# Kernel tuning notes

Hardware: AMD Instinct MI355X
Metric: run time of the kernel (lower is better)

## Reference

```python
import jax, jax.numpy as jnp
import numpy as np

NODE_DIM = 512
HIDDEN = 4096
N_NODES = 4096  # must equal HIDDEN for pool Linear to typecheck (as in source)
N_EDGES = 131072


def setup_inputs() -> dict:
    key = jax.random.key(0)
    ks = jax.random.split(key, 12)
    s1 = 0.02
    x = jax.random.normal(ks[0], (N_NODES, NODE_DIM), dtype=jnp.float32)
    edge_index = jax.random.randint(ks[1], (2, N_EDGES), 0, N_NODES, dtype=jnp.int64)
    # encoder: Linear(node_dim, hidden) -> ReLU -> Linear(hidden, hidden)
    W1 = jax.random.normal(ks[2], (NODE_DIM, HIDDEN), dtype=jnp.float32) * s1
    b1 = jnp.zeros((HIDDEN,), dtype=jnp.float32)
    W2 = jax.random.normal(ks[3], (HIDDEN, HIDDEN), dtype=jnp.float32) * s1
    b2 = jnp.zeros((HIDDEN,), dtype=jnp.float32)
    # pool: Linear(hidden, hidden) -> ReLU -> Linear(hidden, 1)
    W3 = jax.random.normal(ks[4], (HIDDEN, HIDDEN), dtype=jnp.float32) * s1
    b3 = jnp.zeros((HIDDEN,), dtype=jnp.float32)
    W4 = jax.random.normal(ks[5], (HIDDEN, 1), dtype=jnp.float32) * s1
    b4 = jnp.zeros((1,), dtype=jnp.float32)
    return {"x": x, "edge_index": edge_index, "W1": W1, "b1": b1,
            "W2": W2, "b2": b2, "W3": W3, "b3": b3, "W4": W4, "b4": b4}


def reference(x, edge_index, W1, b1, W2, b2, W3, b3, W4, b4):
    # encoder MLP: [N, node_dim] -> [N, hidden]
    h = jax.nn.relu(x @ W1 + b1) @ W2 + b2
    # kernel_vector = (h @ h.T).sum(1) == h @ h.sum(0)  (avoids O(N^2) Gram)
    s = h.sum(axis=0)                 # [hidden]
    kernel_vector = h @ s             # [N]
    kv = kernel_vector[None, :]       # [1, N] with N == hidden
    pooled = jax.nn.relu(kv @ W3 + b3) @ W4 + b4   # [1, 1]
    return pooled
```

## Files before the change

kernel.cpp:

```cpp
#include <hip/hip_runtime.h>

#define NODES 4096
#define NDIM  512
#define HID   4096

typedef __attribute__((ext_vector_type(8))) short bf16x8;
typedef __attribute__((ext_vector_type(4))) float f32x4;

__device__ __forceinline__ float b2f(short v) {
  union { unsigned int u; float f; } c;
  c.u = ((unsigned int)(unsigned short)v) << 16;
  return c.f;
}
__device__ __forceinline__ short f2b(float f) {
  union { float f; unsigned int u; } c; c.f = f;
  unsigned int r = c.u + 0x7fffu + ((c.u >> 16) & 1u);
  return (short)(r >> 16);
}

__global__ __launch_bounds__(256) void k_prep(const float* __restrict__ x,
                                              const float* __restrict__ W1,
                                              const float* __restrict__ b2,
                                              const float* __restrict__ b3,
                                              short* __restrict__ xb,
                                              short* __restrict__ w1t,
                                              float* __restrict__ aacc,
                                              float* __restrict__ svec,
                                              float* __restrict__ uacc) {
  __shared__ float tile[32][33];
  int b = blockIdx.x;
  if (b < 2048) {
    int i = (b * 256 + threadIdx.x) * 4;
    float4 v = *(const float4*)(x + i);
    short4 o;
    o.x = f2b(v.x); o.y = f2b(v.y); o.z = f2b(v.z); o.w = f2b(v.w);
    *(short4*)(xb + i) = o;
  } else if (b < 4096) {
    int t = b - 2048;
    int n0 = (t & 127) * 32;
    int k0 = (t >> 7) * 32;
    int tx = threadIdx.x & 31, ty = threadIdx.x >> 5;
    #pragma unroll
    for (int j = 0; j < 4; ++j) {
      int kk = ty + j * 8;
      tile[kk][tx] = W1[(size_t)(k0 + kk) * HID + n0 + tx];
    }
    __syncthreads();
    #pragma unroll
    for (int j = 0; j < 4; ++j) {
      int nn = ty + j * 8;
      w1t[(size_t)(n0 + nn) * NDIM + k0 + tx] = f2b(tile[tx][nn]);
    }
  } else {
    int j = (b - 4096) * 256 + threadIdx.x;
    aacc[j] = 0.0f;
    svec[j] = (float)NODES * b2[j];
    uacc[j] = b3[j];
  }
}

__global__ __launch_bounds__(512, 2) void k_gemm1(const short* __restrict__ xb,
                                                  const short* __restrict__ w1t,
                                                  const float* __restrict__ b1,
                                                  short* __restrict__ Aout,
                                                  float* __restrict__ colsum) {
  extern __shared__ char smem[];
  __shared__ float csum[256];

  const int tid  = threadIdx.x;
  const int lane = tid & 63;
  const int wid  = tid >> 6;
  const int wr   = wid >> 2;
  const int wc   = wid & 3;

  int bswz = (blockIdx.x & 7) * 32 + (blockIdx.x >> 3);
  const int brow = (bswz >> 4) * 256, bcol = (bswz & 15) * 256;

  f32x4 acc[8][4];
  #pragma unroll
  for (int i = 0; i < 8; ++i)
    #pragma unroll
    for (int j = 0; j < 4; ++j)
      acc[i][j] = (f32x4){0.f, 0.f, 0.f, 0.f};

  if (tid < 256) csum[tid] = 0.f;

  const int fr = lane & 15;
  const int fko = ((lane >> 4) ^ ((lane >> 1) & 3)) * 8;

  const int off0 = tid * 16;
  const int row0 = off0 >> 6;
  const int gs   = (off0 >> 4) & 3;
  const int ce0  = (gs ^ ((row0 >> 1) & 3)) * 8;
  const short* gA0 = xb  + (size_t)(brow + row0) * NDIM + ce0;
  const short* gA1 = xb  + (size_t)(brow + row0 + 128) * NDIM + ce0;
  const short* gB0 = w1t + (size_t)(bcol + row0) * NDIM + ce0;
  const short* gB1 = w1t + (size_t)(bcol + row0 + 128) * NDIM + ce0;

  auto STAGE = [&](int buf, int kt2) {
    char* baseA = smem + buf * 32768;
    char* baseB = smem + 65536 + buf * 32768;
    const int ks = kt2 * 64;
    #pragma unroll
    for (int kh = 0; kh < 2; ++kh) {
      __builtin_amdgcn_global_load_lds(
          (const __attribute__((address_space(1))) void*)(gA0 + ks + kh * 32),
          (__attribute__((address_space(3))) void*)(baseA + kh * 16384 + off0), 16, 0, 0);
      __builtin_amdgcn_global_load_lds(
          (const __attribute__((address_space(1))) void*)(gA1 + ks + kh * 32),
          (__attribute__((address_space(3))) void*)(baseA + kh * 16384 + off0 + 8192), 16, 0, 0);
      __builtin_amdgcn_global_load_lds(
          (const __attribute__((address_space(1))) void*)(gB0 + ks + kh * 32),
          (__attribute__((address_space(3))) void*)(baseB + kh * 16384 + off0), 16, 0, 0);
      __builtin_amdgcn_global_load_lds(
          (const __attribute__((address_space(1))) void*)(gB1 + ks + kh * 32),
          (__attribute__((address_space(3))) void*)(baseB + kh * 16384 + off0 + 8192), 16, 0, 0);
    }
  };

  auto COMPUTE = [&](int buf) {
    #pragma unroll
    for (int kh = 0; kh < 2; ++kh) {
      bf16x8 af[8], bfr[4];
      const short* Ab = (const short*)(smem + buf * 32768 + kh * 16384);
      const short* Bb = (const short*)(smem + 65536 + buf * 32768 + kh * 16384);
      #pragma unroll
      for (int ni = 0; ni < 4; ++ni)
        bfr[ni] = *(const bf16x8*)(Bb + (wc * 64 + ni * 16 + fr) * 32 + fko);
      #pragma unroll
      for (int mi = 0; mi < 8; ++mi)
        af[mi] = *(const bf16x8*)(Ab + (wr * 128 + mi * 16 + fr) * 32 + fko);
      __builtin_amdgcn_s_setprio(1);
      #pragma unroll
      for (int mi = 0; mi < 8; ++mi)
        #pragma unroll
        for (int ni = 0; ni < 4; ++ni)
          acc[mi][ni] = __builtin_amdgcn_mfma_f32_16x16x32_bf16(bfr[ni], af[mi],
                                                                acc[mi][ni], 0, 0, 0);
      __builtin_amdgcn_s_setprio(0);
    }
  };

  STAGE(0, 0);
  #pragma unroll 1
  for (int kt2 = 0; kt2 < NDIM / 64 - 1; ++kt2) {
    STAGE((kt2 + 1) & 1, kt2 + 1);
    asm volatile("s_waitcnt vmcnt(8)" ::: "memory");
    __builtin_amdgcn_s_barrier();
    COMPUTE(kt2 & 1);
    __builtin_amdgcn_s_barrier();
  }
  asm volatile("s_waitcnt vmcnt(0)" ::: "memory");
  __builtin_amdgcn_s_barrier();
  COMPUTE((NDIM / 64 - 1) & 1);

  const int cr = lane & 15;
  const int cg = (lane >> 4) * 4;
  float4 bias4[4];
  #pragma unroll
  for (int ni = 0; ni < 4; ++ni)
    bias4[ni] = *(const float4*)(b1 + bcol + wc * 64 + ni * 16 + cg);

  float cl[4][4];
  #pragma unroll
  for (int ni = 0; ni < 4; ++ni)
    #pragma unroll
    for (int r = 0; r < 4; ++r)
      cl[ni][r] = 0.f;

  short* pk = (short*)smem;
  #pragma unroll 1
  for (int half = 0; half < 2; ++half) {
    __syncthreads();
    if (wr == half) {
      #pragma unroll
      for (int mi = 0; mi < 8; ++mi) {
        int lrow = mi * 16 + cr;
        #pragma unroll
        for (int ni = 0; ni < 4; ++ni) {
          float v0 = fmaxf(acc[mi][ni][0] + bias4[ni].x, 0.f);
          float v1 = fmaxf(acc[mi][ni][1] + bias4[ni].y, 0.f);
          float v2 = fmaxf(acc[mi][ni][2] + bias4[ni].z, 0.f);
          float v3 = fmaxf(acc[mi][ni][3] + bias4[ni].w, 0.f);
          cl[ni][0] += v0; cl[ni][1] += v1; cl[ni][2] += v2; cl[ni][3] += v3;
          short4 o;
          o.x = f2b(v0); o.y = f2b(v1); o.z = f2b(v2); o.w = f2b(v3);
          *(short4*)(pk + lrow * 264 + wc * 64 + ni * 16 + cg) = o;
        }
      }
    }
    __syncthreads();
    #pragma unroll
    for (int i = 0; i < 8; ++i) {
      int c = tid + i * 512;
      int row = c >> 5, ch = c & 31;
      bf16x8 vv = *(const bf16x8*)(pk + row * 264 + ch * 8);
      *(bf16x8*)(Aout + (size_t)(brow + half * 128 + row) * HID + bcol + ch * 8) = vv;
    }
  }

  #pragma unroll
  for (int ni = 0; ni < 4; ++ni)
    #pragma unroll
    for (int r = 0; r < 4; ++r) {
      #pragma unroll
      for (int m = 1; m < 16; m <<= 1)
        cl[ni][r] += __shfl_xor(cl[ni][r], m);
    }
  if (cr == 0) {
    #pragma unroll
    for (int ni = 0; ni < 4; ++ni)
      #pragma unroll
      for (int r = 0; r < 4; ++r)
        atomicAdd(&csum[wc * 64 + ni * 16 + cg + r], cl[ni][r]);
  }
  __syncthreads();
  if (tid < 256) atomicAdd(&colsum[bcol + tid], csum[tid]);
}

__global__ __launch_bounds__(256) void k_gemv_at(const float* __restrict__ W,
                                                 const float* __restrict__ vin,
                                                 float* __restrict__ vout) {
  const int col = blockIdx.x * 1024 + threadIdx.x * 4;
  const int r0  = blockIdx.y * 64;
  float4 accv = {0.f, 0.f, 0.f, 0.f};
  const float* base = W + (size_t)r0 * HID + col;
  #pragma unroll 16
  for (int i = 0; i < 64; ++i) {
    float vi = vin[r0 + i];
    float4 wv = *(const float4*)(base + (size_t)i * HID);
    accv.x += vi * wv.x; accv.y += vi * wv.y;
    accv.z += vi * wv.z; accv.w += vi * wv.w;
  }
  atomicAdd(&vout[col + 0], accv.x);
  atomicAdd(&vout[col + 1], accv.y);
  atomicAdd(&vout[col + 2], accv.z);
  atomicAdd(&vout[col + 3], accv.w);
}

__global__ __launch_bounds__(256) void k_gemv_row(const float* __restrict__ W,
                                                  const float* __restrict__ vin,
                                                  const float* __restrict__ b2,
                                                  float* __restrict__ vout,
                                                  float* __restrict__ beta) {
  __shared__ float red[4];
  if (blockIdx.x == HID / 4) {
    float p = 0.f;
    for (int j = threadIdx.x; j < HID; j += 256) p += b2[j] * vin[j];
    #pragma unroll
    for (int o = 32; o > 0; o >>= 1) p += __shfl_down(p, o);
    int lane = threadIdx.x & 63, w = threadIdx.x >> 6;
    if (lane == 0) red[w] = p;
    __syncthreads();
    if (threadIdx.x == 0) beta[0] = red[0] + red[1] + red[2] + red[3];
    return;
  }
  int w = threadIdx.x >> 6, lane = threadIdx.x & 63;
  int row = blockIdx.x * 4 + w;
  const float* base = W + (size_t)row * HID;
  float p = 0.f;
  #pragma unroll 8
  for (int j = lane * 4; j < HID; j += 256) {
    float4 wv = *(const float4*)(base + j);
    float4 sv = *(const float4*)(vin + j);
    p += wv.x * sv.x + wv.y * sv.y + wv.z * sv.z + wv.w * sv.w;
  }
  #pragma unroll
  for (int o = 32; o > 0; o >>= 1) p += __shfl_down(p, o);
  if (lane == 0) vout[row] = p;
}

__global__ __launch_bounds__(256) void k_kv(const short* __restrict__ A,
                                            const float* __restrict__ t,
                                            const float* __restrict__ beta,
                                            float* __restrict__ kv) {
  int w = threadIdx.x >> 6, lane = threadIdx.x & 63;
  int row = blockIdx.x * 4 + w;
  const short* base = A + (size_t)row * HID;
  float p = 0.f;
  #pragma unroll
  for (int j = lane * 8; j < HID; j += 512) {
    bf16x8 av = *(const bf16x8*)(base + j);
    float4 t0 = *(const float4*)(t + j);
    float4 t1 = *(const float4*)(t + j + 4);
    p += b2f(av[0]) * t0.x + b2f(av[1]) * t0.y + b2f(av[2]) * t0.z + b2f(av[3]) * t0.w
       + b2f(av[4]) * t1.x + b2f(av[5]) * t1.y + b2f(av[6]) * t1.z + b2f(av[7]) * t1.w;
  }
  #pragma unroll
  for (int o = 32; o > 0; o >>= 1) p += __shfl_down(p, o);
  if (lane == 0) kv[row] = p + beta[0];
}

__global__ __launch_bounds__(256) void k_final(const float* __restrict__ uacc,
                                               const float* __restrict__ W4,
                                               const float* __restrict__ b4,
                                               float* __restrict__ out) {
  __shared__ float red[4];
  float p = 0.f;
  for (int j = threadIdx.x; j < HID; j += 256) {
    float uv = uacc[j];
    uv = uv > 0.f ? uv : 0.f;
    p += uv * W4[j];
  }
  #pragma unroll
  for (int o = 32; o > 0; o >>= 1) p += __shfl_down(p, o);
  int lane = threadIdx.x & 63, w = threadIdx.x >> 6;
  if (lane == 0) red[w] = p;
  __syncthreads();
  if (threadIdx.x == 0) out[0] = red[0] + red[1] + red[2] + red[3] + b4[0];
}

extern "C" void kernel_launch(void* const* d_in, const int* in_sizes, int n_in,
                              void* d_out, int out_size, void* d_ws, size_t ws_size,
                              hipStream_t stream) {
  const float* x  = (const float*)d_in[0];
  const float* W1 = (const float*)d_in[2];
  const float* b1 = (const float*)d_in[3];
  const float* W2 = (const float*)d_in[4];
  const float* b2 = (const float*)d_in[5];
  const float* W3 = (const float*)d_in[6];
  const float* b3 = (const float*)d_in[7];
  const float* W4 = (const float*)d_in[8];
  const float* b4 = (const float*)d_in[9];
  float* out = (float*)d_out;

  char* ws = (char*)d_ws;
  short* Abf  = (short*)(ws);
  short* xb   = (short*)(ws + 33554432);
  short* w1t  = (short*)(ws + 37748736);
  float* aacc = (float*)(ws + 41943040);
  float* svec = (float*)(ws + 41959424);
  float* tvec = (float*)(ws + 41975808);
  float* kvv  = (float*)(ws + 41992192);
  float* uacc = (float*)(ws + 42008576);
  float* beta = (float*)(ws + 42024960);

  k_prep    <<<dim3(4112),     dim3(256), 0, stream>>>(x, W1, b2, b3, xb, w1t, aacc, svec, uacc);
  k_gemm1   <<<dim3(256),      dim3(512), 131072, stream>>>(xb, w1t, b1, Abf, aacc);
  k_gemv_at <<<dim3(4, 64),    dim3(256), 0, stream>>>(W2, aacc, svec);
  k_gemv_row<<<dim3(1025),     dim3(256), 0, stream>>>(W2, svec, b2, tvec, beta);
  k_kv      <<<dim3(1024),     dim3(256), 0, stream>>>(Abf, tvec, beta, kvv);
  k_gemv_at <<<dim3(4, 64),    dim3(256), 0, stream>>>(W3, kvv, uacc);
  k_final   <<<dim3(1),        dim3(256), 0, stream>>>(uacc, W4, b4, out);
}
```

Baseline: 95.09 us.

## Restructure GEMM1 main loop into finer-grained half-tile pipelined schedule

Replaces the per-tile double-buffered stage/compute loop with a schedule that issues global-to-LDS loads per K-half and splits the MFMA work into four sub-phases. Each sub-phase has its own LDS fragment loads, barriers and vmcnt waits. The aim is to overlap loads with compute more tightly and to cut register pressure by holding only 4 A fragments at a time. In exchange it adds many more barriers and lgkmcnt waits per iteration, which could serialize the waves.

```diff
diff --git a/kernel.cpp b/kernel.cpp
--- a/kernel.cpp
+++ b/kernel.cpp
@@ -97,62 +97,87 @@
   const short* gB0 = w1t + (size_t)(bcol + row0) * NDIM + ce0;
   const short* gB1 = w1t + (size_t)(bcol + row0 + 128) * NDIM + ce0;
 
-  auto STAGE = [&](int buf, int kt2) {
-    char* baseA = smem + buf * 32768;
-    char* baseB = smem + 65536 + buf * 32768;
-    const int ks = kt2 * 64;
-    #pragma unroll
-    for (int kh = 0; kh < 2; ++kh) {
-      __builtin_amdgcn_global_load_lds(
-          (const __attribute__((address_space(1))) void*)(gA0 + ks + kh * 32),
-          (__attribute__((address_space(3))) void*)(baseA + kh * 16384 + off0), 16, 0, 0);
-      __builtin_amdgcn_global_load_lds(
-          (const __attribute__((address_space(1))) void*)(gA1 + ks + kh * 32),
-          (__attribute__((address_space(3))) void*)(baseA + kh * 16384 + off0 + 8192), 16, 0, 0);
-      __builtin_amdgcn_global_load_lds(
-          (const __attribute__((address_space(1))) void*)(gB0 + ks + kh * 32),
-          (__attribute__((address_space(3))) void*)(baseB + kh * 16384 + off0), 16, 0, 0);
-      __builtin_amdgcn_global_load_lds(
-          (const __attribute__((address_space(1))) void*)(gB1 + ks + kh * 32),
-          (__attribute__((address_space(3))) void*)(baseB + kh * 16384 + off0 + 8192), 16, 0, 0);
-    }
-  };
-
-  auto COMPUTE = [&](int buf) {
-    #pragma unroll
-    for (int kh = 0; kh < 2; ++kh) {
-      bf16x8 af[8], bfr[4];
-      const short* Ab = (const short*)(smem + buf * 32768 + kh * 16384);
-      const short* Bb = (const short*)(smem + 65536 + buf * 32768 + kh * 16384);
-      #pragma unroll
-      for (int ni = 0; ni < 4; ++ni)
-        bfr[ni] = *(const bf16x8*)(Bb + (wc * 64 + ni * 16 + fr) * 32 + fko);
-      #pragma unroll
-      for (int mi = 0; mi < 8; ++mi)
-        af[mi] = *(const bf16x8*)(Ab + (wr * 128 + mi * 16 + fr) * 32 + fko);
-      __builtin_amdgcn_s_setprio(1);
-      #pragma unroll
-      for (int mi = 0; mi < 8; ++mi)
-        #pragma unroll
-        for (int ni = 0; ni < 4; ++ni)
-          acc[mi][ni] = __builtin_amdgcn_mfma_f32_16x16x32_bf16(bfr[ni], af[mi],
-                                                                acc[mi][ni], 0, 0, 0);
-      __builtin_amdgcn_s_setprio(0);
-    }
-  };
-
-  STAGE(0, 0);
+#define GLOAD(src, dst) __builtin_amdgcn_global_load_lds( \
+    (const __attribute__((address_space(1))) void*)(src), \
+    (__attribute__((address_space(3))) void*)(dst), 16, 0, 0)
+
+#define STAGE_HALF(buf, tile_, kh) do { \
+    char* bA_ = smem + (buf) * 32768 + (kh) * 16384; \
+    char* bB_ = smem + 65536 + (buf) * 32768 + (kh) * 16384; \
+    int ks_ = (tile_) * 64 + (kh) * 32; \
+    GLOAD(gA0 + ks_, bA_ + off0); \
+    GLOAD(gA1 + ks_, bA_ + off0 + 8192); \
+    GLOAD(gB0 + ks_, bB_ + off0); \
+    GLOAD(gB1 + ks_, bB_ + off0 + 8192); \
+  } while (0)
+
+#define DS_BFR(buf, kh) do { \
+    const short* Bb_ = (const short*)(smem + 65536 + (buf) * 32768 + (kh) * 16384); \
+    _Pragma("unroll") \
+    for (int ni = 0; ni < 4; ++ni) \
+      bfr[ni] = *(const bf16x8*)(Bb_ + (wc * 64 + ni * 16 + fr) * 32 + fko); \
+  } while (0)
+
+#define DS_AF(buf, kh, mh) do { \
+    const short* Ab_ = (const short*)(smem + (buf) * 32768 + (kh) * 16384); \
+    _Pragma("unroll") \
+    for (int mi = 0; mi < 4; ++mi) \
+      af[mi] = *(const bf16x8*)(Ab_ + (wr * 128 + ((mh) * 4 + mi) * 16 + fr) * 32 + fko); \
+  } while (0)
+
+#define MFMA16(mh) do { \
+    __builtin_amdgcn_s_setprio(1); \
+    _Pragma("unroll") \
+    for (int mi = 0; mi < 4; ++mi) \
+      _Pragma("unroll") \
+      for (int ni = 0; ni < 4; ++ni) \
+        acc[(mh) * 4 + mi][ni] = __builtin_amdgcn_mfma_f32_16x16x32_bf16( \
+            bfr[ni], af[mi], acc[(mh) * 4 + mi][ni], 0, 0, 0); \
+    __builtin_amdgcn_s_setprio(0); \
+  } while (0)
+
+#define BAR() __builtin_amdgcn_s_barrier()
+#define LGKM0() asm volatile("s_waitcnt lgkmcnt(0)" ::: "memory")
+#define WCNT(s) asm volatile("s_waitcnt " s ::: "memory")
+
+#define ITER(kk, DO_S0, DO_S2, V1, V3) do { \
+    int b_ = (kk) & 1; \
+    bf16x8 af[4], bfr[4]; \
+     \
+    if (DO_S0) STAGE_HALF(((kk) + 1) & 1, (kk) + 1, 1); \
+    DS_BFR(b_, 0); DS_AF(b_, 0, 0); \
+    BAR(); LGKM0(); \
+    MFMA16(0); \
+    BAR(); \
+     \
+    DS_AF(b_, 0, 1); \
+    BAR(); LGKM0(); \
+    MFMA16(1); \
+    WCNT(V1); BAR(); \
+     \
+    if (DO_S2) STAGE_HALF(b_, (kk) + 2, 0); \
+    DS_BFR(b_, 1); DS_AF(b_, 1, 0); \
+    BAR(); LGKM0(); \
+    MFMA16(0); \
+    BAR(); \
+     \
+    DS_AF(b_, 1, 1); \
+    BAR(); LGKM0(); \
+    MFMA16(1); \
+    WCNT(V3); BAR(); \
+  } while (0)
+
+  STAGE_HALF(0, 0, 0);
+  STAGE_HALF(0, 0, 1);
+  STAGE_HALF(1, 1, 0);
+  WCNT("vmcnt(8)");
+  BAR();
+
   #pragma unroll 1
-  for (int kt2 = 0; kt2 < NDIM / 64 - 1; ++kt2) {
-    STAGE((kt2 + 1) & 1, kt2 + 1);
-    asm volatile("s_waitcnt vmcnt(8)" ::: "memory");
-    __builtin_amdgcn_s_barrier();
-    COMPUTE(kt2 & 1);
-    __builtin_amdgcn_s_barrier();
-  }
-  asm volatile("s_waitcnt vmcnt(0)" ::: "memory");
-  __builtin_amdgcn_s_barrier();
-  COMPUTE((NDIM / 64 - 1) & 1);
+  for (int kt = 0; kt < 6; ++kt)
+    ITER(kt, true, true, "vmcnt(8)", "vmcnt(8)");
+  ITER(6, true, false, "vmcnt(8)", "vmcnt(4)");
+  ITER(7, false, false, "vmcnt(0)", "vmcnt(0)");
 
   const int cr = lane & 15;
   const int cg = (lane >> 4) * 4;
```

After: 92.86 us. 1.02x faster.
